# Kernel tuning notes

Measured on AMD Instinct MI355X. Metric: run time of the kernel, lower is better.

The kernel has to match this reference:

```python
import jax, jax.numpy as jnp
import numpy as np
import math

B, S, D, H = 8, 1024, 1024, 16
DH = D // H  # 64


def setup_inputs() -> dict:
    key = jax.random.key(0)
    ks = jax.random.split(key, 10)
    inputs = jax.random.normal(ks[0], (B, S, D), dtype=jnp.float32)
    mask = jax.random.randint(ks[1], (B, S, S), 0, 2) == 1  # bool [B,S,S]
    sc = 1.0 / math.sqrt(D)
    # per-head projection weights stacked: [H, D, DH], biases [H, DH]
    Wq = jax.random.normal(ks[2], (H, D, DH), dtype=jnp.float32) * sc
    bq = jax.random.normal(ks[3], (H, DH), dtype=jnp.float32) * 0.02
    Wk = jax.random.normal(ks[4], (H, D, DH), dtype=jnp.float32) * sc
    bk = jax.random.normal(ks[5], (H, DH), dtype=jnp.float32) * 0.02
    Wv = jax.random.normal(ks[6], (H, D, DH), dtype=jnp.float32) * sc
    bv = jax.random.normal(ks[7], (H, DH), dtype=jnp.float32) * 0.02
    Wo = jax.random.normal(ks[8], (D, D), dtype=jnp.float32) * sc
    bo = jax.random.normal(ks[9], (D,), dtype=jnp.float32) * 0.02
    return {"inputs": inputs, "mask": mask, "Wq": Wq, "bq": bq, "Wk": Wk,
            "bk": bk, "Wv": Wv, "bv": bv, "Wo": Wo, "bo": bo}


def reference(inputs, mask, Wq, bq, Wk, bk, Wv, bv, Wo, bo):
    d_model = inputs.shape[-1]
    scale = 1.0 / jnp.sqrt(jnp.asarray(d_model, inputs.dtype))  # note: sqrt(d_model), as in source
    # batched per-head projections: [B,H,S,DH]
    Q = jnp.einsum('bsd,hde->bhse', inputs, Wq) + bq[None, :, None, :]
    K = jnp.einsum('bsd,hde->bhse', inputs, Wk) + bk[None, :, None, :]
    V = jnp.einsum('bsd,hde->bhse', inputs, Wv) + bv[None, :, None, :]
    scores = jnp.einsum('bhse,bhte->bhst', Q, K) * scale  # [B,H,S,S]
    scores = jnp.where(mask[:, None, :, :], jnp.asarray(-1e9, scores.dtype), scores)
    attn = jax.nn.softmax(scores, axis=-1)
    ctx = jnp.einsum('bhst,bhte->bhse', attn, V)  # [B,H,S,DH]
    # concat heads along last dim (head h -> slice h*DH:(h+1)*DH), matches torch.cat
    bsz, h, s, dh = ctx.shape
    x = ctx.transpose(0, 2, 1, 3).reshape(bsz, s, h * dh)
    return x @ Wo + bo
```

## Files before the change

kernel.cpp:

```cpp
#include <hip/hip_runtime.h>
#include <hip/hip_bf16.h>
#include <stdint.h>


typedef __attribute__((ext_vector_type(8))) short short8;
typedef __attribute__((ext_vector_type(4))) float floatx4;

__device__ __forceinline__ int swz(int r, int kc) { return r * 8 + (kc ^ (r & 7)); }
__device__ __forceinline__ short8 as_frag(uint4 u) { return __builtin_bit_cast(short8, u); }
__device__ __forceinline__ floatx4 mfma16(short8 a, short8 b, floatx4 c) {
    return __builtin_amdgcn_mfma_f32_16x16x32_bf16(a, b, c, 0, 0, 0);
}
__device__ __forceinline__ unsigned short f2bu(float f) {
    return __builtin_bit_cast(unsigned short, __float2bfloat16(f));
}
__device__ __forceinline__ short f2b(float f) {
    return __builtin_bit_cast(short, __float2bfloat16(f));
}
__device__ __forceinline__ float b2f(short s) {
    return __bfloat162float(__builtin_bit_cast(__hip_bfloat16, s));
}
__device__ __forceinline__ void dma16(const void* g, void* l) {
    __builtin_amdgcn_global_load_lds(
        (const __attribute__((address_space(1))) uint32_t*)g,
        (__attribute__((address_space(3))) uint32_t*)l, 16, 0, 0);
}
__device__ __forceinline__ uint2 pack4(float a, float b, float c, float d) {
    uint2 p;
    p.x = (unsigned)f2bu(a) | ((unsigned)f2bu(b) << 16);
    p.y = (unsigned)f2bu(c) | ((unsigned)f2bu(d) << 16);
    return p;
}

__device__ __forceinline__ void detect_mode(const unsigned* Xw, int* s_is32) {
    if (threadIdx.x < 64) {
        unsigned lo = Xw[threadIdx.x] & 0xFFFFu;
        unsigned e = (lo >> 7) & 0xFFu;
        unsigned long long bal = __ballot(e >= 88u && e <= 150u);
        if (threadIdx.x == 0) *s_is32 = (bal != ~0ull) ? 1 : 0;
    }
    __syncthreads();
}

__device__ __forceinline__ float load_elt(const void* p, size_t idx, int is32) {
    return is32 ? ((const float*)p)[idx]
                : __bfloat162float(((const __hip_bfloat16*)p)[idx]);
}

__global__ __launch_bounds__(256) void prep_all(
    const void* __restrict__ Wq, const void* __restrict__ Wk,
    const void* __restrict__ Wv, const void* __restrict__ Wo,
    const void* __restrict__ bq, const void* __restrict__ bk,
    const void* __restrict__ bv, const void* __restrict__ bo,
    const void* __restrict__ mask_raw, const void* __restrict__ X,
    __hip_bfloat16* __restrict__ WT, __hip_bfloat16* __restrict__ WoT,
    __hip_bfloat16* __restrict__ bc, unsigned long long* __restrict__ bits64,
    __hip_bfloat16* __restrict__ Xb, int do_x)
{
    __shared__ __hip_bfloat16 T[64][72];
    __shared__ int s_is32;
    int blk = blockIdx.x;
    int tid = threadIdx.x;
    const unsigned* Xw = (const unsigned*)X;

    if (blk < 1024) {
        detect_mode(Xw, &s_is32);
        const void* src; size_t src_off;
        __hip_bfloat16* dst;
        int src_ld, dst_ld;
        if (blk < 768) {
            int p = blk >> 8;
            int rem = blk & 255;
            int h = rem >> 4, dt = rem & 15;
            src = (p == 0) ? Wq : (p == 1) ? Wk : Wv;
            src_off = ((size_t)h * 1024 + (size_t)dt * 64) * 64;
            dst = WT + (((size_t)p * 16 + h) * 64) * 1024 + dt * 64;
            src_ld = 64; dst_ld = 1024;
        } else {
            int t = blk - 768;
            int kt = t >> 4, nt = t & 15;
            src = Wo; src_off = (size_t)kt * 64 * 1024 + nt * 64;
            dst = WoT + (size_t)nt * 64 * 1024 + kt * 64;
            src_ld = 1024; dst_ld = 1024;
        }
        #pragma unroll
        for (int i = 0; i < 16; i++) {
            int idx = tid + i * 256;
            int r = idx >> 6, c = idx & 63;
            T[c][r] = __float2bfloat16(load_elt(src, src_off + (size_t)r * src_ld + c, s_is32));
        }
        __syncthreads();
        #pragma unroll
        for (int i = 0; i < 16; i++) {
            int idx = tid + i * 256;
            int r = idx >> 6, c = idx & 63;
            dst[(size_t)r * dst_ld + c] = T[r][c];
        }
    } else if (blk == 1024) {
        detect_mode(Xw, &s_is32);
        #pragma unroll
        for (int i = 0; i < 16; i++) {
            int idx = tid + i * 256;
            int which = idx >> 10, j = idx & 1023;
            const void* src = (which == 0) ? bq : (which == 1) ? bk : (which == 2) ? bv : bo;
            bc[idx] = __float2bfloat16(load_elt(src, j, s_is32));
        }
    } else if (blk < 1537) {
        int blkL = blk - 1025;
        const int* mi = (const int*)mask_raw;
        const unsigned char* mb = (const unsigned char*)mask_raw;
        int lane = tid & 63;
        bool ok = true;
        #pragma unroll
        for (int i = 0; i < 4; i++) {
            unsigned v = (unsigned)mi[lane * 4 + i];
            if (v > 1u) ok = false;
        }
        bool is_i32 = (__ballot(ok) == ~0ull);
        int gw = (blkL * 256 + tid) >> 6;
        const int NW = 512 * 4;
        const int NWORDS = (8 * 1024 * 1024) / 64;
        if (is_i32) {
            for (int i = gw; i < NWORDS; i += NW) {
                int mv = mi[(size_t)i * 64 + lane];
                unsigned long long bal = __ballot(mv != 0);
                if (lane == 0) bits64[i] = bal;
            }
        } else {
            for (int i = gw; i < NWORDS; i += NW) {
                int mv = mb[(size_t)i * 64 + lane];
                unsigned long long bal = __ballot(mv != 0);
                if (lane == 0) bits64[i] = bal;
            }
        }
    } else if (do_x) {
        detect_mode(Xw, &s_is32);
        int blkL = blk - 1537;
        size_t g = ((size_t)blkL * 256 + tid) * 16;
        if (s_is32) {
            const float* Xf = (const float*)X;
            #pragma unroll
            for (int half = 0; half < 2; half++) {
                float4 f0 = *(const float4*)(Xf + g + half * 8);
                float4 f1 = *(const float4*)(Xf + g + half * 8 + 4);
                short8 s;
                s[0] = f2b(f0.x); s[1] = f2b(f0.y); s[2] = f2b(f0.z); s[3] = f2b(f0.w);
                s[4] = f2b(f1.x); s[5] = f2b(f1.y); s[6] = f2b(f1.z); s[7] = f2b(f1.w);
                *(uint4*)(Xb + g + half * 8) = __builtin_bit_cast(uint4, s);
            }
        } else {
            const uint4* Xu = (const uint4*)X;
            *(uint4*)(Xb + g)     = Xu[g / 8];
            *(uint4*)(Xb + g + 8) = Xu[g / 8 + 1];
        }
    }
}

__global__ __launch_bounds__(256, 2) void qkv_gemm_dma(
    const __hip_bfloat16* __restrict__ Xb,
    const __hip_bfloat16* __restrict__ WT,
    const __hip_bfloat16* __restrict__ bc,
    __hip_bfloat16* __restrict__ Q,
    __hip_bfloat16* __restrict__ Ko,
    __hip_bfloat16* __restrict__ Vt)
{
    __shared__ uint4 AsU[256 * 8];
    __shared__ uint4 BsU[128 * 8];
    int tid = threadIdx.x, lane = tid & 63, wave = tid >> 6;
    int quad = lane >> 4, ln = lane & 15;
    int mw = wave & 1, nw = wave >> 1;
    int m0 = blockIdx.x * 256;
    int n0 = blockIdx.y * 128;
    const __hip_bfloat16* Wp = WT + (size_t)n0 * 1024;

    floatx4 acc[8][4];
    #pragma unroll
    for (int i = 0; i < 8; i++)
        #pragma unroll
        for (int j = 0; j < 4; j++) acc[i][j] = (floatx4){0.f, 0.f, 0.f, 0.f};

    for (int k0 = 0; k0 < 1024; k0 += 64) {
        #pragma unroll
        for (int i = 0; i < 8; i++) {
            int r = wave * 64 + i * 8 + (lane >> 3);
            int kc = (lane & 7) ^ (r & 7);
            char* lds = (char*)AsU + (size_t)(wave * 512 + i * 64) * 16;
            dma16(Xb + (size_t)(m0 + r) * 1024 + k0 + kc * 8, lds);
        }
        #pragma unroll
        for (int i = 0; i < 4; i++) {
            int r = wave * 32 + i * 8 + (lane >> 3);
            int kc = (lane & 7) ^ (r & 7);
            char* lds = (char*)BsU + (size_t)(wave * 256 + i * 64) * 16;
            dma16(Wp + (size_t)r * 1024 + k0 + kc * 8, lds);
        }
        __syncthreads();
        #pragma unroll
        for (int kk = 0; kk < 2; kk++) {
            short8 af[8], bf[4];
            #pragma unroll
            for (int mi = 0; mi < 8; mi++)
                af[mi] = as_frag(AsU[swz(mw * 128 + mi * 16 + ln, kk * 4 + quad)]);
            #pragma unroll
            for (int ni = 0; ni < 4; ni++)
                bf[ni] = as_frag(BsU[swz(nw * 64 + ni * 16 + ln, kk * 4 + quad)]);
            #pragma unroll
            for (int mi = 0; mi < 8; mi++)
                #pragma unroll
                for (int ni = 0; ni < 4; ni++)
                    acc[mi][ni] = mfma16(af[mi], bf[ni], acc[mi][ni]);
        }
        __syncthreads();
    }

    int b = m0 >> 10;
    int s0 = m0 & 1023;
    int proj = n0 >> 10;
    if (proj == 2) {
        #pragma unroll
        for (int ni = 0; ni < 4; ni++) {
            int n = n0 + nw * 64 + ni * 16 + ln;
            int h = (n >> 6) & 15, e = n & 63;
            float bval = __bfloat162float(bc[2 * 1024 + (n & 1023)]);
            #pragma unroll
            for (int mi = 0; mi < 8; mi++) {
                int sb = s0 + mw * 128 + mi * 16 + quad * 4;
                uint2 pk = pack4(acc[mi][ni][0] + bval, acc[mi][ni][1] + bval,
                                 acc[mi][ni][2] + bval, acc[mi][ni][3] + bval);
                *(uint2*)(Vt + (((size_t)b * 16 + h) * 64 + e) * 1024 + sb) = pk;
            }
        }
    } else {
        __hip_bfloat16* P = (proj == 0) ? Q : Ko;
        #pragma unroll
        for (int ni = 0; ni < 4; ni++) {
            int n = n0 + nw * 64 + ni * 16 + ln;
            int h = (n >> 6) & 15, e = n & 63;
            float bval = __bfloat162float(bc[proj * 1024 + (n & 1023)]);
            #pragma unroll
            for (int mi = 0; mi < 8; mi++) {
                #pragma unroll
                for (int r = 0; r < 4; r++) {
                    int s = s0 + mw * 128 + mi * 16 + quad * 4 + r;
                    P[(((size_t)b * 16 + h) * 1024 + s) * 64 + e] =
                        __float2bfloat16(acc[mi][ni][r] + bval);
                }
            }
        }
    }
}

__global__ __launch_bounds__(256) void qkv_gemm2(
    const void* __restrict__ Xsrc,
    const __hip_bfloat16* __restrict__ WT,
    const __hip_bfloat16* __restrict__ bc,
    __hip_bfloat16* __restrict__ Q,
    __hip_bfloat16* __restrict__ Ko,
    __hip_bfloat16* __restrict__ Vt)
{
    __shared__ int s_is32;
    detect_mode((const unsigned*)Xsrc, &s_is32);
    __shared__ uint4 AsU[128 * 8];
    __shared__ uint4 BsU[128 * 8];
    int tid = threadIdx.x, lane = tid & 63, wave = tid >> 6;
    int quad = lane >> 4, ln = lane & 15;
    int m0 = blockIdx.x * 128;
    int n0 = blockIdx.y * 128;
    const __hip_bfloat16* Wp = WT + (size_t)n0 * 1024;
    const float* Xf = (const float*)Xsrc;
    const __hip_bfloat16* Xh = (const __hip_bfloat16*)Xsrc;

    floatx4 acc[2][8];
    #pragma unroll
    for (int i = 0; i < 2; i++)
        #pragma unroll
        for (int j = 0; j < 8; j++) acc[i][j] = (floatx4){0.f, 0.f, 0.f, 0.f};

    for (int k0 = 0; k0 < 1024; k0 += 64) {
        if (s_is32) {
            #pragma unroll
            for (int i = 0; i < 4; i++) {
                int id = tid + i * 256;
                int r = id >> 3, kc = id & 7;
                size_t off = (size_t)(m0 + r) * 1024 + k0 + kc * 8;
                float4 f0 = *(const float4*)(Xf + off);
                float4 f1 = *(const float4*)(Xf + off + 4);
                short8 s;
                s[0] = f2b(f0.x); s[1] = f2b(f0.y); s[2] = f2b(f0.z); s[3] = f2b(f0.w);
                s[4] = f2b(f1.x); s[5] = f2b(f1.y); s[6] = f2b(f1.z); s[7] = f2b(f1.w);
                AsU[swz(r, kc)] = __builtin_bit_cast(uint4, s);
            }
        } else {
            #pragma unroll
            for (int i = 0; i < 4; i++) {
                int id = tid + i * 256;
                int r = id >> 3, kc = id & 7;
                AsU[swz(r, kc)] = *(const uint4*)(Xh + (size_t)(m0 + r) * 1024 + k0 + kc * 8);
            }
        }
        #pragma unroll
        for (int i = 0; i < 4; i++) {
            int id = tid + i * 256;
            int r = id >> 3, kc = id & 7;
            BsU[swz(r, kc)] = *(const uint4*)(Wp + (size_t)r * 1024 + k0 + kc * 8);
        }
        __syncthreads();
        #pragma unroll
        for (int kk = 0; kk < 2; kk++) {
            short8 a0 = as_frag(AsU[swz(wave * 32 + ln, kk * 4 + quad)]);
            short8 a1 = as_frag(AsU[swz(wave * 32 + 16 + ln, kk * 4 + quad)]);
            #pragma unroll
            for (int nt = 0; nt < 8; nt++) {
                short8 bf = as_frag(BsU[swz(nt * 16 + ln, kk * 4 + quad)]);
                acc[0][nt] = mfma16(a0, bf, acc[0][nt]);
                acc[1][nt] = mfma16(a1, bf, acc[1][nt]);
            }
        }
        __syncthreads();
    }

    int b = m0 >> 10;
    int s0 = m0 & 1023;
    #pragma unroll
    for (int nt = 0; nt < 8; nt++) {
        int n = n0 + nt * 16 + ln;
        int proj = n >> 10, h = (n >> 6) & 15, e = n & 63;
        float bval = __bfloat162float(bc[proj * 1024 + (n & 1023)]);
        #pragma unroll
        for (int mt = 0; mt < 2; mt++) {
            #pragma unroll
            for (int r = 0; r < 4; r++) {
                int s = s0 + wave * 32 + mt * 16 + quad * 4 + r;
                float v = acc[mt][nt][r] + bval;
                if (proj == 2) {
                    Vt[(((size_t)b * 16 + h) * 64 + e) * 1024 + s] = __float2bfloat16(v);
                } else {
                    __hip_bfloat16* P = (proj == 0) ? Q : Ko;
                    P[(((size_t)b * 16 + h) * 1024 + s) * 64 + e] = __float2bfloat16(v);
                }
            }
        }
    }
}

__global__ __launch_bounds__(128) void attn(
    const __hip_bfloat16* __restrict__ Q,
    const __hip_bfloat16* __restrict__ K,
    const __hip_bfloat16* __restrict__ Vt,
    const unsigned long long* __restrict__ bits,
    __hip_bfloat16* __restrict__ ctx)
{
    __shared__ uint4 QsU[128 * 8];
    __shared__ uint4 KsU[64 * 8];
    __shared__ uint4 VsU[64 * 8];
    __shared__ uint4 PsU[2 * 64 * 8];
    __shared__ unsigned long long Ms[128];

    int tid = threadIdx.x, lane = tid & 63, w = tid >> 6;
    int quad = lane >> 4, ln = lane & 15;
    int bh = blockIdx.x;
    int q0 = blockIdx.y * 128;
    int b = bh >> 4, h = bh & 15;
    const __hip_bfloat16* Qp = Q + (size_t)bh * 1024 * 64;
    const __hip_bfloat16* Kp = K + (size_t)bh * 1024 * 64;
    const __hip_bfloat16* Vp = Vt + (size_t)bh * 64 * 1024;
    const unsigned long long* bp = bits + (size_t)b * 1024 * 16;

    #pragma unroll
    for (int i = 0; i < 8; i++) {
        int r = w * 64 + i * 8 + (lane >> 3);
        int kc = (lane & 7) ^ (r & 7);
        char* lds = (char*)QsU + (size_t)(w * 512 + i * 64) * 16;
        dma16(Qp + (size_t)(q0 + r) * 64 + kc * 8, lds);
    }
    __syncthreads();
    short8 qf[4][2];
    #pragma unroll
    for (int g = 0; g < 4; g++)
        #pragma unroll
        for (int kk = 0; kk < 2; kk++)
            qf[g][kk] = as_frag(QsU[swz(w * 64 + g * 16 + ln, kk * 4 + quad)]);

    floatx4 acc_o[4][4];
    #pragma unroll
    for (int g = 0; g < 4; g++)
        #pragma unroll
        for (int i = 0; i < 4; i++) acc_o[g][i] = (floatx4){0.f, 0.f, 0.f, 0.f};
    float lsum[4] = {0.f, 0.f, 0.f, 0.f};
    const float scale = 0.03125f;
    __hip_bfloat16* Pw = (__hip_bfloat16*)&PsU[w * 512];

    for (int t0 = 0; t0 < 1024; t0 += 64) {
        __syncthreads();
        #pragma unroll
        for (int i = 0; i < 4; i++) {
            int r = w * 32 + i * 8 + (lane >> 3);
            int kc = (lane & 7) ^ (r & 7);
            char* ldsK = (char*)KsU + (size_t)(w * 256 + i * 64) * 16;
            char* ldsV = (char*)VsU + (size_t)(w * 256 + i * 64) * 16;
            dma16(Kp + (size_t)(t0 + r) * 64 + kc * 8, ldsK);
            dma16(Vp + (size_t)r * 1024 + t0 + kc * 8, ldsV);
        }
        Ms[tid] = bp[(size_t)(q0 + tid) * 16 + (t0 >> 6)];
        __syncthreads();

        floatx4 st[4][4];
        #pragma unroll
        for (int g = 0; g < 4; g++)
            #pragma unroll
            for (int i = 0; i < 4; i++) st[g][i] = (floatx4){0.f, 0.f, 0.f, 0.f};
        #pragma unroll
        for (int kk = 0; kk < 2; kk++) {
            #pragma unroll
            for (int tt = 0; tt < 4; tt++) {
                short8 kf = as_frag(KsU[swz(tt * 16 + ln, kk * 4 + quad)]);
                #pragma unroll
                for (int g = 0; g < 4; g++)
                    st[g][tt] = mfma16(kf, qf[g][kk], st[g][tt]);
            }
        }

        #pragma unroll
        for (int g = 0; g < 4; g++) {
            int qloc = g * 16 + ln;
            unsigned long long mw = Ms[w * 64 + qloc];
            #pragma unroll
            for (int tt = 0; tt < 4; tt++) {
                unsigned mb = (unsigned)(mw >> (tt * 16 + quad * 4)) & 0xFu;
                float pe0 = (mb & 1u) ? 0.f : __expf(st[g][tt][0] * scale);
                float pe1 = (mb & 2u) ? 0.f : __expf(st[g][tt][1] * scale);
                float pe2 = (mb & 4u) ? 0.f : __expf(st[g][tt][2] * scale);
                float pe3 = (mb & 8u) ? 0.f : __expf(st[g][tt][3] * scale);
                lsum[g] += (pe0 + pe1) + (pe2 + pe3);
                int kc = tt * 2 + (quad >> 1);
                int off = qloc * 64 + (kc ^ (qloc & 7)) * 8 + (quad & 1) * 4;
                *(uint2*)(Pw + off) = pack4(pe0, pe1, pe2, pe3);
            }
        }

        #pragma unroll
        for (int kk = 0; kk < 2; kk++) {
            short8 pf[4];
            #pragma unroll
            for (int g = 0; g < 4; g++)
                pf[g] = as_frag(PsU[w * 512 + swz(g * 16 + ln, kk * 4 + quad)]);
            #pragma unroll
            for (int et = 0; et < 4; et++) {
                short8 vf = as_frag(VsU[swz(et * 16 + ln, kk * 4 + quad)]);
                #pragma unroll
                for (int g = 0; g < 4; g++)
                    acc_o[g][et] = mfma16(vf, pf[g], acc_o[g][et]);
            }
        }
    }

    #pragma unroll
    for (int g = 0; g < 4; g++) {
        lsum[g] += __shfl_xor(lsum[g], 16, 64);
        lsum[g] += __shfl_xor(lsum[g], 32, 64);
    }

    #pragma unroll
    for (int g = 0; g < 4; g++) {
        float inv = 1.f / fmaxf(lsum[g], 1e-20f);
        int s = q0 + w * 64 + g * 16 + ln;
        __hip_bfloat16* crow = ctx + ((size_t)b * 1024 + s) * 1024 + h * 64 + quad * 4;
        #pragma unroll
        for (int et = 0; et < 4; et++) {
            uint2 pk = pack4(acc_o[g][et][0] * inv, acc_o[g][et][1] * inv,
                             acc_o[g][et][2] * inv, acc_o[g][et][3] * inv);
            *(uint2*)(crow + et * 16) = pk;
        }
    }
}

__global__ __launch_bounds__(256) void out_gemm_dma(
    const __hip_bfloat16* __restrict__ Cx,
    const __hip_bfloat16* __restrict__ WoT,
    const __hip_bfloat16* __restrict__ bc,
    const unsigned* __restrict__ Xw,
    void* __restrict__ dout,
    int direct)
{
    __shared__ int s_is32;
    detect_mode(Xw, &s_is32);
    __shared__ uint4 AsU[128 * 8];
    __shared__ uint4 BsU[128 * 8];
    int tid = threadIdx.x, lane = tid & 63, wave = tid >> 6;
    int quad = lane >> 4, ln = lane & 15;
    int mw = wave & 1, nw = wave >> 1;
    int m0 = blockIdx.x * 128;
    int n0 = blockIdx.y * 128;

    floatx4 acc[4][4];
    #pragma unroll
    for (int i = 0; i < 4; i++)
        #pragma unroll
        for (int j = 0; j < 4; j++) acc[i][j] = (floatx4){0.f, 0.f, 0.f, 0.f};

    for (int k0 = 0; k0 < 1024; k0 += 64) {
        #pragma unroll
        for (int i = 0; i < 4; i++) {
            int r = wave * 32 + i * 8 + (lane >> 3);
            int kc = (lane & 7) ^ (r & 7);
            char* ldsA = (char*)AsU + (size_t)(wave * 256 + i * 64) * 16;
            char* ldsB = (char*)BsU + (size_t)(wave * 256 + i * 64) * 16;
            dma16(Cx + (size_t)(m0 + r) * 1024 + k0 + kc * 8, ldsA);
            dma16(WoT + (size_t)(n0 + r) * 1024 + k0 + kc * 8, ldsB);
        }
        __syncthreads();
        #pragma unroll
        for (int kk = 0; kk < 2; kk++) {
            short8 af[4], bf[4];
            #pragma unroll
            for (int mi = 0; mi < 4; mi++)
                af[mi] = as_frag(AsU[swz(mw * 64 + mi * 16 + ln, kk * 4 + quad)]);
            #pragma unroll
            for (int ni = 0; ni < 4; ni++)
                bf[ni] = as_frag(BsU[swz(nw * 64 + ni * 16 + ln, kk * 4 + quad)]);
            #pragma unroll
            for (int mi = 0; mi < 4; mi++)
                #pragma unroll
                for (int ni = 0; ni < 4; ni++)
                    acc[mi][ni] = mfma16(af[mi], bf[ni], acc[mi][ni]);
        }
        __syncthreads();
    }

    const __hip_bfloat16* bo = bc + 3 * 1024;
    #pragma unroll
    for (int ni = 0; ni < 4; ni++) {
        int n = n0 + nw * 64 + ni * 16 + ln;
        float bval = __bfloat162float(bo[n]);
        #pragma unroll
        for (int mi = 0; mi < 4; mi++) {
            #pragma unroll
            for (int r = 0; r < 4; r++) {
                int m = m0 + mw * 64 + mi * 16 + quad * 4 + r;
                float v = acc[mi][ni][r] + bval;
                if (direct && s_is32) ((float*)dout)[(size_t)m * 1024 + n] = v;
                else ((__hip_bfloat16*)dout)[(size_t)m * 1024 + n] = __float2bfloat16(v);
            }
        }
    }
}

__global__ __launch_bounds__(256) void emit_out(
    const __hip_bfloat16* __restrict__ Fo, const unsigned* __restrict__ Xw,
    void* __restrict__ dout)
{
    __shared__ int s_is32;
    detect_mode(Xw, &s_is32);
    size_t g = (size_t)blockIdx.x * 256 + threadIdx.x;
    uint4 u = *(const uint4*)(Fo + g * 8);
    if (s_is32) {
        short8 s = __builtin_bit_cast(short8, u);
        float4 f0, f1;
        f0.x = b2f(s[0]); f0.y = b2f(s[1]); f0.z = b2f(s[2]); f0.w = b2f(s[3]);
        f1.x = b2f(s[4]); f1.y = b2f(s[5]); f1.z = b2f(s[6]); f1.w = b2f(s[7]);
        *(float4*)((float*)dout + g * 8) = f0;
        *(float4*)((float*)dout + g * 8 + 4) = f1;
    } else {
        *(uint4*)((__hip_bfloat16*)dout + g * 8) = u;
    }
}

extern "C" void kernel_launch(void* const* d_in, const int* in_sizes, int n_in,
                              void* d_out, int out_size, void* d_ws, size_t ws_size,
                              hipStream_t stream) {
    const void* X  = d_in[0];
    const void* mk = d_in[1];
    const void* Wq = d_in[2];
    const void* bq = d_in[3];
    const void* Wk = d_in[4];
    const void* bk = d_in[5];
    const void* Wv = d_in[6];
    const void* bv = d_in[7];
    const void* Wo = d_in[8];
    const void* bo = d_in[9];
    const unsigned* Xw = (const unsigned*)X;

    char* ws = (char*)d_ws;
    __hip_bfloat16*     WT   = (__hip_bfloat16*)(ws);
    __hip_bfloat16*     WoT  = (__hip_bfloat16*)(ws + ((size_t)6 << 20));
    unsigned long long* bits = (unsigned long long*)(ws + ((size_t)8 << 20));
    __hip_bfloat16*     bc   = (__hip_bfloat16*)(ws + ((size_t)9 << 20));
    __hip_bfloat16*     Xb   = (__hip_bfloat16*)(ws + ((size_t)10 << 20));
    __hip_bfloat16*     Qb   = (__hip_bfloat16*)(ws + ((size_t)26 << 20));
    __hip_bfloat16*     Kb   = (__hip_bfloat16*)(ws + ((size_t)42 << 20));
    __hip_bfloat16*     Vtb  = (__hip_bfloat16*)(ws + ((size_t)58 << 20));

    bool bigws = ws_size >= ((size_t)74 << 20);

    hipLaunchKernelGGL(prep_all, dim3(3585), dim3(256), 0, stream,
                       Wq, Wk, Wv, Wo, bq, bk, bv, bo, mk, X,
                       WT, WoT, bc, bits, Xb, bigws ? 1 : 0);

    if (bigws) {
        __hip_bfloat16* Cx = Xb;
        hipLaunchKernelGGL(qkv_gemm_dma, dim3(32, 24), dim3(256), 0, stream,
                           Xb, WT, bc, Qb, Kb, Vtb);
        hipLaunchKernelGGL(attn, dim3(128, 8), dim3(128), 0, stream,
                           Qb, Kb, Vtb, bits, Cx);
        hipLaunchKernelGGL(out_gemm_dma, dim3(64, 8), dim3(256), 0, stream,
                           Cx, WoT, bc, Xw, d_out, 1);
    } else {
        __hip_bfloat16* Cx = (__hip_bfloat16*)d_out;
        __hip_bfloat16* Fo = Qb;
        hipLaunchKernelGGL(qkv_gemm2, dim3(64, 24), dim3(256), 0, stream,
                           X, WT, bc, Qb, Kb, Vtb);
        hipLaunchKernelGGL(attn, dim3(128, 8), dim3(128), 0, stream,
                           Qb, Kb, Vtb, bits, Cx);
        hipLaunchKernelGGL(out_gemm_dma, dim3(64, 8), dim3(256), 0, stream,
                           Cx, WoT, bc, Xw, (void*)Fo, 0);
        hipLaunchKernelGGL(emit_out, dim3(4096), dim3(256), 0, stream,
                           Fo, Xw, d_out);
    }
}
```

Baseline: 343.8 us.

## Split attention block across four waves with 32 query rows each

The attention kernel now runs 256 threads (four waves), each owning 32 query rows instead of 64, so per-wave accumulators and fragments shrink. The Q tile no longer goes through LDS; each lane loads its Q fragments straight from global memory. Launch bounds request four blocks per CU to raise occupancy and hide latency. In exchange, each K/V tile staged in LDS feeds fewer MFMAs per wave, and there are more waves taking part in every barrier.

```diff
diff --git a/kernel.cpp b/kernel.cpp
--- a/kernel.cpp
+++ b/kernel.cpp
@@ -343,17 +343,16 @@
     }
 }
 
-__global__ __launch_bounds__(128) void attn(
+__global__ __launch_bounds__(256, 4) void attn(
     const __hip_bfloat16* __restrict__ Q,
     const __hip_bfloat16* __restrict__ K,
     const __hip_bfloat16* __restrict__ Vt,
     const unsigned long long* __restrict__ bits,
     __hip_bfloat16* __restrict__ ctx)
 {
-    __shared__ uint4 QsU[128 * 8];
     __shared__ uint4 KsU[64 * 8];
     __shared__ uint4 VsU[64 * 8];
-    __shared__ uint4 PsU[2 * 64 * 8];
+    __shared__ uint4 PsU[4 * 256];
     __shared__ unsigned long long Ms[128];
 
     int tid = threadIdx.x, lane = tid & 63, w = tid >> 6;
@@ -366,47 +365,41 @@
     const __hip_bfloat16* Vp = Vt + (size_t)bh * 64 * 1024;
     const unsigned long long* bp = bits + (size_t)b * 1024 * 16;
 
-    #pragma unroll
-    for (int i = 0; i < 8; i++) {
-        int r = w * 64 + i * 8 + (lane >> 3);
-        int kc = (lane & 7) ^ (r & 7);
-        char* lds = (char*)QsU + (size_t)(w * 512 + i * 64) * 16;
-        dma16(Qp + (size_t)(q0 + r) * 64 + kc * 8, lds);
-    }
-    __syncthreads();
-    short8 qf[4][2];
-    #pragma unroll
-    for (int g = 0; g < 4; g++)
+    short8 qf[2][2];
+    #pragma unroll
+    for (int g = 0; g < 2; g++)
         #pragma unroll
         for (int kk = 0; kk < 2; kk++)
-            qf[g][kk] = as_frag(QsU[swz(w * 64 + g * 16 + ln, kk * 4 + quad)]);
-
-    floatx4 acc_o[4][4];
-    #pragma unroll
-    for (int g = 0; g < 4; g++)
+            qf[g][kk] = as_frag(*(const uint4*)(
+                Qp + (size_t)(q0 + w * 32 + g * 16 + ln) * 64 + kk * 32 + quad * 8));
+
+    floatx4 acc_o[2][4];
+    #pragma unroll
+    for (int g = 0; g < 2; g++)
         #pragma unroll
         for (int i = 0; i < 4; i++) acc_o[g][i] = (floatx4){0.f, 0.f, 0.f, 0.f};
-    float lsum[4] = {0.f, 0.f, 0.f, 0.f};
+    float lsum[2] = {0.f, 0.f};
     const float scale = 0.03125f;
-    __hip_bfloat16* Pw = (__hip_bfloat16*)&PsU[w * 512];
+    __hip_bfloat16* Pw = (__hip_bfloat16*)&PsU[w * 256];
 
     for (int t0 = 0; t0 < 1024; t0 += 64) {
         __syncthreads();
         #pragma unroll
-        for (int i = 0; i < 4; i++) {
-            int r = w * 32 + i * 8 + (lane >> 3);
+        for (int i = 0; i < 2; i++) {
+            int r = w * 16 + i * 8 + (lane >> 3);
             int kc = (lane & 7) ^ (r & 7);
-            char* ldsK = (char*)KsU + (size_t)(w * 256 + i * 64) * 16;
-            char* ldsV = (char*)VsU + (size_t)(w * 256 + i * 64) * 16;
+            char* ldsK = (char*)KsU + (size_t)(w * 128 + i * 64) * 16;
+            char* ldsV = (char*)VsU + (size_t)(w * 128 + i * 64) * 16;
             dma16(Kp + (size_t)(t0 + r) * 64 + kc * 8, ldsK);
             dma16(Vp + (size_t)r * 1024 + t0 + kc * 8, ldsV);
         }
-        Ms[tid] = bp[(size_t)(q0 + tid) * 16 + (t0 >> 6)];
-        __syncthreads();
-
-        floatx4 st[4][4];
-        #pragma unroll
-        for (int g = 0; g < 4; g++)
+        if (tid < 128)
+            Ms[tid] = bp[(size_t)(q0 + tid) * 16 + (t0 >> 6)];
+        __syncthreads();
+
+        floatx4 st[2][4];
+        #pragma unroll
+        for (int g = 0; g < 2; g++)
             #pragma unroll
             for (int i = 0; i < 4; i++) st[g][i] = (floatx4){0.f, 0.f, 0.f, 0.f};
         #pragma unroll
@@ -414,16 +407,15 @@
             #pragma unroll
             for (int tt = 0; tt < 4; tt++) {
                 short8 kf = as_frag(KsU[swz(tt * 16 + ln, kk * 4 + quad)]);
-                #pragma unroll
-                for (int g = 0; g < 4; g++)
-                    st[g][tt] = mfma16(kf, qf[g][kk], st[g][tt]);
-            }
-        }
-
-        #pragma unroll
-        for (int g = 0; g < 4; g++) {
+                st[0][tt] = mfma16(kf, qf[0][kk], st[0][tt]);
+                st[1][tt] = mfma16(kf, qf[1][kk], st[1][tt]);
+            }
+        }
+
+        #pragma unroll
+        for (int g = 0; g < 2; g++) {
             int qloc = g * 16 + ln;
-            unsigned long long mw = Ms[w * 64 + qloc];
+            unsigned long long mw = Ms[w * 32 + qloc];
             #pragma unroll
             for (int tt = 0; tt < 4; tt++) {
                 unsigned mb = (unsigned)(mw >> (tt * 16 + quad * 4)) & 0xFu;
@@ -440,30 +432,27 @@
 
         #pragma unroll
         for (int kk = 0; kk < 2; kk++) {
-            short8 pf[4];
-            #pragma unroll
-            for (int g = 0; g < 4; g++)
-                pf[g] = as_frag(PsU[w * 512 + swz(g * 16 + ln, kk * 4 + quad)]);
+            short8 pf0 = as_frag(PsU[w * 256 + swz(0 * 16 + ln, kk * 4 + quad)]);
+            short8 pf1 = as_frag(PsU[w * 256 + swz(1 * 16 + ln, kk * 4 + quad)]);
             #pragma unroll
             for (int et = 0; et < 4; et++) {
                 short8 vf = as_frag(VsU[swz(et * 16 + ln, kk * 4 + quad)]);
-                #pragma unroll
-                for (int g = 0; g < 4; g++)
-                    acc_o[g][et] = mfma16(vf, pf[g], acc_o[g][et]);
-            }
-        }
-    }
-
-    #pragma unroll
-    for (int g = 0; g < 4; g++) {
+                acc_o[0][et] = mfma16(vf, pf0, acc_o[0][et]);
+                acc_o[1][et] = mfma16(vf, pf1, acc_o[1][et]);
+            }
+        }
+    }
+
+    #pragma unroll
+    for (int g = 0; g < 2; g++) {
         lsum[g] += __shfl_xor(lsum[g], 16, 64);
         lsum[g] += __shfl_xor(lsum[g], 32, 64);
     }
 
     #pragma unroll
-    for (int g = 0; g < 4; g++) {
+    for (int g = 0; g < 2; g++) {
         float inv = 1.f / fmaxf(lsum[g], 1e-20f);
-        int s = q0 + w * 64 + g * 16 + ln;
+        int s = q0 + w * 32 + g * 16 + ln;
         __hip_bfloat16* crow = ctx + ((size_t)b * 1024 + s) * 1024 + h * 64 + quad * 4;
         #pragma unroll
         for (int et = 0; et < 4; et++) {
@@ -600,7 +589,7 @@
         __hip_bfloat16* Cx = Xb;
         hipLaunchKernelGGL(qkv_gemm_dma, dim3(32, 24), dim3(256), 0, stream,
                            Xb, WT, bc, Qb, Kb, Vtb);
-        hipLaunchKernelGGL(attn, dim3(128, 8), dim3(128), 0, stream,
+        hipLaunchKernelGGL(attn, dim3(128, 8), dim3(256), 0, stream,
                            Qb, Kb, Vtb, bits, Cx);
         hipLaunchKernelGGL(out_gemm_dma, dim3(64, 8), dim3(256), 0, stream,
                            Cx, WoT, bc, Xw, d_out, 1);
@@ -609,7 +598,7 @@
         __hip_bfloat16* Fo = Qb;
         hipLaunchKernelGGL(qkv_gemm2, dim3(64, 24), dim3(256), 0, stream,
                            X, WT, bc, Qb, Kb, Vtb);
-        hipLaunchKernelGGL(attn, dim3(128, 8), dim3(128), 0, stream,
+        hipLaunchKernelGGL(attn, dim3(128, 8), dim3(256), 0, stream,
                            Qb, Kb, Vtb, bits, Cx);
         hipLaunchKernelGGL(out_gemm_dma, dim3(64, 8), dim3(256), 0, stream,
                            Cx, WoT, bc, Xw, (void*)Fo, 0);
```

Result: faster. 307.4 us (-10.6%).
